# Performance work log

Hardware: AMD Instinct MI355X
Metric: run time of the kernel (lower is better)

Reference implementation:

```python
import jax, jax.numpy as jnp
import numpy as np

CELL = 0.5          # grid_map cell size (meters)
NUM_POSES = 256     # config.num_pose_samples


def setup_inputs() -> dict:
    key = jax.random.key(0)
    k1, k2, k3, k4 = jax.random.split(key, 4)
    B, N, I, J, D = 2, 1024, 128, 128, 32
    f_q = jax.random.normal(k1, (B, N, D), jnp.float32)
    f_map = jax.random.normal(k2, (B, I, J, D), jnp.float32)
    # query frustum points: 32x32 grid, x in [-15.5, 15.5], y in [0.5, 31.5]
    xs = jnp.arange(32, dtype=jnp.float32) - 15.5
    ys = jnp.arange(32, dtype=jnp.float32) + 0.5
    grid = jnp.stack(jnp.meshgrid(xs, ys, indexing='ij'), -1).reshape(-1, 2)
    q_xy = jnp.broadcast_to(grid, (B, N, 2)).astype(jnp.float32)
    valid_q = jax.random.bernoulli(k3, 0.9, (B, N))
    valid_map = jax.random.bernoulli(k4, 0.8, (B, I, J))
    temperature = jnp.array(0.5, jnp.float32)
    return {"f_q": f_q, "f_map": f_map, "q_xy": q_xy, "temperature": temperature,
            "valid_q": valid_q, "valid_map": valid_map, "seed": 0}


def reference(f_q, f_map, q_xy, temperature, valid_q, valid_map, seed):
    B, N, D = f_q.shape
    _, I, J, _ = f_map.shape
    K = NUM_POSES

    # dense cross-correlation: [B, N, I, J]
    sim = jnp.einsum('bnd,bijd->bnij', f_q, f_map)
    sim = jax.nn.relu(sim)                      # clip_negative_scores
    sim = sim.astype(jnp.float32) * jnp.exp(temperature)
    # joint softmax over the two spatial axes
    m = sim.max(axis=(-2, -1), keepdims=True)
    e = jnp.exp(sim - m)
    prob = e / e.sum(axis=(-2, -1), keepdims=True)
    num_valid = valid_q.sum(-1).clip(min=1).astype(jnp.float32)[:, None, None, None]
    sim = sim / num_valid
    prob = prob / num_valid

    # --- RANSAC 2-point pose sampling (no gradient through prob) ---
    p = jax.lax.stop_gradient(prob)
    kq, km = jax.random.split(jax.random.key(seed))
    n_idx = jax.random.randint(kq, (B, 2 * K), 0, N)          # 2 query pts per pose
    b_idx = jnp.arange(B)[:, None]
    p_flat = p.reshape(B, N, I * J)
    rows = p_flat[b_idx, n_idx]                               # [B, 2K, IJ]
    m_flat = jax.random.categorical(km, jnp.log(rows + 1e-20), axis=-1)  # [B, 2K]
    mi, mj = m_flat // J, m_flat % J
    m_xy = (jnp.stack([mi, mj], -1).astype(jnp.float32) + 0.5) * CELL    # cell centers
    m_xy = m_xy.reshape(B, K, 2, 2)
    q_pts = q_xy[b_idx, n_idx].reshape(B, K, 2, 2)
    dq = q_pts[:, :, 1] - q_pts[:, :, 0]
    dm = m_xy[:, :, 1] - m_xy[:, :, 0]
    theta = jnp.arctan2(dm[..., 1], dm[..., 0]) - jnp.arctan2(dq[..., 1], dq[..., 0])
    c, s = jnp.cos(theta), jnp.sin(theta)
    R = jnp.stack([jnp.stack([c, -s], -1), jnp.stack([s, c], -1)], -2)   # [B,K,2,2]
    t = m_xy[:, :, 0] - jnp.einsum('bkxy,bky->bkx', R, q_pts[:, :, 0])   # [B,K,2]

    # --- score every pose hypothesis ---
    p_map = jnp.einsum('bkxy,bny->bknx', R, q_xy) + t[:, :, None]        # [B,K,N,2]
    ij = jnp.floor(p_map / CELL).astype(jnp.int32)
    inb = (ij[..., 0] >= 0) & (ij[..., 0] < I) & (ij[..., 1] >= 0) & (ij[..., 1] < J)
    flat = jnp.clip(ij[..., 0], 0, I - 1) * J + jnp.clip(ij[..., 1], 0, J - 1)  # [B,K,N]
    vmap_flat = valid_map.reshape(B, I * J)
    vgather = vmap_flat[b_idx, flat.reshape(B, K * N)].reshape(B, K, N)
    sim_flat = sim.reshape(B, N, I * J)
    sgather = jnp.take_along_axis(sim_flat, flat.transpose(0, 2, 1), axis=2)  # [B,N,K]
    mask = valid_q[:, None, :] & inb & vgather                                # [B,K,N]
    scores = jnp.sum(sgather.transpose(0, 2, 1) * mask, axis=-1)              # [B,K]
    return scores
```

## Files before the change

### kernel.cpp

```cpp
#include <hip/hip_runtime.h>
#include <hip/hip_bf16.h>
#include <stdint.h>

typedef unsigned int u32;
typedef _Float16 f16x8 __attribute__((ext_vector_type(8)));
typedef float f32x4 __attribute__((ext_vector_type(4)));

#define IJ 16384
#define NQ 1024
#define NB 2
#define KP 256
#define NSEG 8
#define SEGW 2048

__device__ __forceinline__ void tf2x32(u32 k0, u32 k1, u32& x0, u32& x1) {
  u32 kx = k0 ^ k1 ^ 0x1BD11BDAu;
#define TFR(r) { x0 += x1; x1 = (x1 << (r)) | (x1 >> (32 - (r))); x1 ^= x0; }
  x0 += k0; x1 += k1;
  TFR(13) TFR(15) TFR(26) TFR(6)
  x0 += k1; x1 += kx + 1u;
  TFR(17) TFR(29) TFR(16) TFR(24)
  x0 += kx; x1 += k0 + 2u;
  TFR(13) TFR(15) TFR(26) TFR(6)
  x0 += k0; x1 += k1 + 3u;
  TFR(17) TFR(29) TFR(16) TFR(24)
  x0 += k1; x1 += kx + 4u;
  TFR(13) TFR(15) TFR(26) TFR(6)
  x0 += kx; x1 += k0 + 5u;
#undef TFR
}

__device__ __forceinline__ void tf_subkey(u32 k0, u32 k1, u32 i, u32& s0, u32& s1) {
  u32 x0 = 0u, x1 = i;
  tf2x32(k0, k1, x0, x1);
  s0 = x0; s1 = x1;
}

__device__ __forceinline__ u32 tf_xorbits(u32 k0, u32 k1, u32 i) {
  u32 x0 = 0u, x1 = i;
  tf2x32(k0, k1, x0, x1);
  return x0 ^ x1;
}

__device__ __forceinline__ void derive_keys(int seed, u32& kq0, u32& kq1,
                                            u32& km0, u32& km1) {
  u32 k0 = 0u;
  u32 k1 = (u32)seed;
  tf_subkey(k0, k1, 0u, kq0, kq1);
  tf_subkey(k0, k1, 1u, km0, km1);
}

__device__ __forceinline__ float gumbel_from_bits(u32 w) {
  const float tiny = 1.17549435e-38f;
  float fl = __uint_as_float((w >> 9) | 0x3f800000u) - 1.0f;
  float u = fl * (1.0f - tiny) + tiny;
  u = fmaxf(tiny, u);
  return -logf(-logf(u));
}

__device__ __forceinline__ bool read_bool(const void* p, int idx, int is32) {
  return is32 ? (((const int*)p)[idx] != 0)
              : (((const unsigned char*)p)[idx] != 0);
}

__global__ void setup_kernel(const void* __restrict__ valid_q,
                             const int* __restrict__ seedp,
                             float* __restrict__ row_max,
                             float* __restrict__ num_valid,
                             int* __restrict__ n_idx,
                             int* __restrict__ bool_is32) {
  __shared__ int sred[256];
  __shared__ int is32_s;
  const int blk = blockIdx.x, tid = threadIdx.x;
  if (blk < 4) {
    int s = blk * 256 + tid;
    u32 kq0, kq1, km0, km1;
    derive_keys(seedp[0], kq0, kq1, km0, km1);
    u32 l0, l1;
    tf_subkey(kq0, kq1, 1u, l0, l1);
    u32 w = tf_xorbits(l0, l1, (u32)s);
    n_idx[s] = (int)(w & 1023u);
  } else if (blk == 4) {
    const unsigned char* vb = (const unsigned char*)valid_q;
    int ones = 0;
    for (int i = tid; i < 2048; i += 256) ones += (vb[i] == 1) ? 1 : 0;
    sred[tid] = ones;
    __syncthreads();
    for (int off = 128; off > 0; off >>= 1) {
      if (tid < off) sred[tid] += sred[tid + off];
      __syncthreads();
    }
    if (tid == 0) {
      is32_s = (sred[0] < 1152) ? 1 : 0;
      bool_is32[0] = is32_s;
    }
    __syncthreads();
    const int is32 = is32_s;
    for (int b = 0; b < 2; ++b) {
      int acc = 0;
      for (int i = tid; i < NQ; i += 256)
        acc += read_bool(valid_q, b * NQ + i, is32) ? 1 : 0;
      sred[tid] = acc;
      __syncthreads();
      for (int off = 128; off > 0; off >>= 1) {
        if (tid < off) sred[tid] += sred[tid + off];
        __syncthreads();
      }
      if (tid == 0) {
        float nv = (float)sred[0];
        num_valid[b] = nv < 1.f ? 1.f : nv;
      }
      __syncthreads();
    }
  } else {
    for (int i = (blk - 5) * 256 + tid; i < NB * NQ; i += 768) row_max[i] = 0.f;
  }
}

__global__ __launch_bounds__(256) void gemm_kernel(
    const float* __restrict__ f_q, const float* __restrict__ f_map,
    const float* __restrict__ temp, float* __restrict__ sim,
    float* __restrict__ row_max, float* __restrict__ rowsum_part) {
  __shared__ __align__(16) _Float16 ldsA[2][4][64][8];
  __shared__ __align__(16) _Float16 ldsB[2][16][64][8];
  const int tid = threadIdx.x;
  const int b = blockIdx.z;
  const int n0 = blockIdx.y * 64;
  const int ij0 = blockIdx.x * 256;

  {
    const int l = tid & 63, rt = tid >> 6;
    const int g = l >> 4, r = l & 15;
    const float* src = f_q + ((size_t)b * NQ + n0 + rt * 16 + r) * 32 + g * 4;
    float4 v0 = *(const float4*)src;
    float4 v1 = *(const float4*)(src + 16);
    float x[8] = {v0.x, v0.y, v0.z, v0.w, v1.x, v1.y, v1.z, v1.w};
    f16x8 h1, h2;
#pragma unroll
    for (int e = 0; e < 8; ++e) {
      _Float16 a = (_Float16)x[e];
      h1[e] = a;
      h2[e] = (_Float16)((x[e] - (float)a) * 2048.0f);
    }
    *(f16x8*)(&ldsA[0][rt][l][0]) = h1;
    *(f16x8*)(&ldsA[1][rt][l][0]) = h2;
  }
  for (int s = tid; s < 1024; s += 256) {
    const int l = s & 63, t = s >> 6;
    const int g = l >> 4, r = l & 15;
    const float* src = f_map + ((size_t)b * IJ + ij0 + t * 16 + r) * 32 + g * 4;
    float4 v0 = *(const float4*)src;
    float4 v1 = *(const float4*)(src + 16);
    float x[8] = {v0.x, v0.y, v0.z, v0.w, v1.x, v1.y, v1.z, v1.w};
    f16x8 h1, h2;
#pragma unroll
    for (int e = 0; e < 8; ++e) {
      _Float16 a = (_Float16)x[e];
      h1[e] = a;
      h2[e] = (_Float16)((x[e] - (float)a) * 2048.0f);
    }
    *(f16x8*)(&ldsB[0][t][l][0]) = h1;
    *(f16x8*)(&ldsB[1][t][l][0]) = h2;
  }
  __syncthreads();

  const int w = tid >> 6, l = tid & 63;
  const f16x8 q1 = *(const f16x8*)(&ldsA[0][w][l][0]);
  const f16x8 q2 = *(const f16x8*)(&ldsA[1][w][l][0]);
  const f32x4 zero4 = {0.f, 0.f, 0.f, 0.f};
  const float c11 = 4.8828125e-4f;
  f32x4 acc[16];
#pragma unroll
  for (int t = 0; t < 16; ++t) {
    f16x8 m1 = *(const f16x8*)(&ldsB[0][t][l][0]);
    f16x8 m2 = *(const f16x8*)(&ldsB[1][t][l][0]);
    f32x4 x = __builtin_amdgcn_mfma_f32_16x16x32_f16(m2, q2, zero4, 0, 0, 0);
    x *= c11;
    x = __builtin_amdgcn_mfma_f32_16x16x32_f16(m2, q1, x, 0, 0, 0);
    x = __builtin_amdgcn_mfma_f32_16x16x32_f16(m1, q2, x, 0, 0, 0);
    x *= c11;
    acc[t] = __builtin_amdgcn_mfma_f32_16x16x32_f16(m1, q1, x, 0, 0, 0);
  }

  const float et = expf(temp[0]);
  const int r15 = l & 15, g = l >> 4;
  const int row = n0 + w * 16 + r15;
  float* base = sim + ((size_t)b * NQ + row) * IJ + ij0 + g * 4;
  float rm = 0.f, se = 0.f;
#pragma unroll
  for (int t = 0; t < 16; ++t) {
    float4 o;
    o.x = fmaxf(acc[t][0], 0.f) * et;
    o.y = fmaxf(acc[t][1], 0.f) * et;
    o.z = fmaxf(acc[t][2], 0.f) * et;
    o.w = fmaxf(acc[t][3], 0.f) * et;
    *(float4*)(base + t * 16) = o;
    rm = fmaxf(rm, fmaxf(fmaxf(o.x, o.y), fmaxf(o.z, o.w)));
    se += expf(o.x); se += expf(o.y); se += expf(o.z); se += expf(o.w);
  }
#pragma unroll
  for (int off = 16; off < 64; off <<= 1) {
    se += __shfl_xor(se, off, 64);
    rm = fmaxf(rm, __shfl_xor(rm, off, 64));
  }
  if (g == 0) {
    rowsum_part[((size_t)(b * NQ + row)) * 64 + blockIdx.x] = se;
    atomicMax((u32*)&row_max[(size_t)b * NQ + row], __float_as_uint(rm));
  }
}

__global__ void sumexp_reduce_kernel(const float* __restrict__ rowsum_part,
                                     const float* __restrict__ row_max,
                                     float* __restrict__ row_sumexp) {
  const int row = blockIdx.x * 256 + threadIdx.x;
  if (row >= NB * NQ) return;
  const float* p = rowsum_part + (size_t)row * 64;
  float s = 0.f;
#pragma unroll
  for (int t = 0; t < 64; ++t) s += p[t];
  row_sumexp[row] = s * expf(-row_max[row]);
}

__global__ __launch_bounds__(256) void cat_seg_kernel(
    const float* __restrict__ sim, const float* __restrict__ row_max,
    const float* __restrict__ row_sumexp, const float* __restrict__ num_valid,
    const int* __restrict__ n_idx, const int* __restrict__ seedp,
    float* __restrict__ segv, int* __restrict__ segi) {
  __shared__ unsigned short cand[2][SEGW];
  __shared__ int ccount[2];
  __shared__ u32 keys[2];
  __shared__ float sv[2][256];
  __shared__ int si[2][256];
  const int seg = blockIdx.x;
  const int t = blockIdx.y;
  const int tid = threadIdx.x;
  if (tid == 0) {
    u32 kq0, kq1, km0, km1;
    derive_keys(seedp[0], kq0, kq1, km0, km1);
    keys[0] = km0; keys[1] = km1;
    ccount[0] = 0; ccount[1] = 0;
  }
  __syncthreads();

  const int nA = n_idx[t], nB = n_idx[512 + t];
  const float m0 = row_max[nA], s0 = row_sumexp[nA];
  const float m1 = row_max[NQ + nB], s1 = row_sumexp[NQ + nB];
  const float nv0 = num_valid[0], nv1 = num_valid[1];
  const float thA = m0 - 25.0f;
  const float thB = m1 - 25.0f;
  const float* r0 = sim + (size_t)nA * IJ + seg * SEGW;
  const float* r1 = sim + (size_t)(NQ + nB) * IJ + seg * SEGW;

#pragma unroll
  for (int k = 0; k < 2; ++k) {
    const int l = tid + k * 256;
    const int lf = l * 4;
    float4 va = ((const float4*)r0)[l];
    float4 vb = ((const float4*)r1)[l];
    const float ra[4] = {va.x, va.y, va.z, va.w};
    const float rb[4] = {vb.x, vb.y, vb.z, vb.w};
#pragma unroll
    for (int c = 0; c < 4; ++c) {
      if (ra[c] > thA) { int p = atomicAdd(&ccount[0], 1); cand[0][p] = (unsigned short)(lf + c); }
      if (rb[c] > thB) { int p = atomicAdd(&ccount[1], 1); cand[1][p] = (unsigned short)(lf + c); }
    }
  }
  __syncthreads();

  const u32 km0 = keys[0], km1 = keys[1];
  const int c0 = ccount[0], c1 = ccount[1];
  const int fbase = seg * SEGW;
  float bv0 = -1e30f, bv1 = -1e30f;
  int bi0 = IJ, bi1 = IJ;
  for (int c = tid; c < c0; c += 256) {
    int f = fbase + (int)cand[0][c];
    u32 w = tf_xorbits(km0, km1, (u32)(t * IJ + f));
    float g = gumbel_from_bits(w);
    float e = expf(r0[f - fbase] - m0);
    float v = logf((e / s0) / nv0 + 1e-20f) + g;
    if (v > bv0 || (v == bv0 && f < bi0)) { bv0 = v; bi0 = f; }
  }
  for (int c = tid; c < c1; c += 256) {
    int f = fbase + (int)cand[1][c];
    u32 w = tf_xorbits(km0, km1, (u32)(t * IJ + f) + 8388608u);
    float g = gumbel_from_bits(w);
    float e = expf(r1[f - fbase] - m1);
    float v = logf((e / s1) / nv1 + 1e-20f) + g;
    if (v > bv1 || (v == bv1 && f < bi1)) { bv1 = v; bi1 = f; }
  }
  sv[0][tid] = bv0; si[0][tid] = bi0;
  sv[1][tid] = bv1; si[1][tid] = bi1;
  __syncthreads();
  for (int off = 128; off > 0; off >>= 1) {
    if (tid < off) {
#pragma unroll
      for (int q = 0; q < 2; ++q) {
        float v2 = sv[q][tid + off];
        int i2 = si[q][tid + off];
        if (v2 > sv[q][tid] || (v2 == sv[q][tid] && i2 < si[q][tid])) {
          sv[q][tid] = v2; si[q][tid] = i2;
        }
      }
    }
    __syncthreads();
  }
  if (tid == 0) {
    segv[(0 * 512 + t) * NSEG + seg] = sv[0][0];
    segi[(0 * 512 + t) * NSEG + seg] = si[0][0];
    segv[(1 * 512 + t) * NSEG + seg] = sv[1][0];
    segi[(1 * 512 + t) * NSEG + seg] = si[1][0];
  }
}

__global__ void cat_reduce_kernel(const float* __restrict__ segv,
                                  const int* __restrict__ segi,
                                  int* __restrict__ m_flat) {
  const int idx = blockIdx.x * 256 + threadIdx.x;
  if (idx >= NB * 512) return;
  float bv = -1e30f;
  int bi = IJ;
#pragma unroll
  for (int s = 0; s < NSEG; ++s) {
    float v = segv[idx * NSEG + s];
    int i = segi[idx * NSEG + s];
    if (v > bv || (v == bv && i < bi)) { bv = v; bi = i; }
  }
  m_flat[idx] = bi;
}

__global__ void pose_kernel(const float* __restrict__ q_xy,
                            const int* __restrict__ n_idx,
                            const int* __restrict__ m_flat,
                            float4* __restrict__ poses) {
  const int idx = blockIdx.x * 256 + threadIdx.x;
  if (idx >= NB * KP) return;
  const int b = idx >> 8, k = idx & 255;
  const int t0 = b * 512 + 2 * k, t1 = t0 + 1;
  const int na = n_idx[t0], nb = n_idx[t1];
  const float2 q0 = ((const float2*)q_xy)[(size_t)b * NQ + na];
  const float2 q1 = ((const float2*)q_xy)[(size_t)b * NQ + nb];
  const int ma = m_flat[t0], mb = m_flat[t1];
  const float m0x = ((float)(ma >> 7) + 0.5f) * 0.5f;
  const float m0y = ((float)(ma & 127) + 0.5f) * 0.5f;
  const float m1x = ((float)(mb >> 7) + 0.5f) * 0.5f;
  const float m1y = ((float)(mb & 127) + 0.5f) * 0.5f;
  const float dqx = q1.x - q0.x, dqy = q1.y - q0.y;
  const float dmx = m1x - m0x, dmy = m1y - m0y;
  const float theta = atan2f(dmy, dmx) - atan2f(dqy, dqx);
  const float c = cosf(theta), s = sinf(theta);
  const float tx = m0x - (c * q0.x - s * q0.y);
  const float ty = m0y - (s * q0.x + c * q0.y);
  poses[idx] = make_float4(c, s, tx, ty);
}

__global__ __launch_bounds__(256) void score_kernel(
    const float* __restrict__ sim, const float* __restrict__ q_xy,
    const void* __restrict__ valid_q, const void* __restrict__ valid_map,
    const float* __restrict__ num_valid, const float4* __restrict__ poses,
    const int* __restrict__ bool_is32, float* __restrict__ out) {
  __shared__ float sred[256];
  const int idx = blockIdx.x;
  const int tid = threadIdx.x;
  const int b = idx >> 8;
  const int is32 = bool_is32[0];
  const float4 P = poses[idx];
  float acc = 0.f;
  for (int n = tid; n < NQ; n += 256) {
    float2 q = ((const float2*)q_xy)[(size_t)b * NQ + n];
    float px = P.x * q.x - P.y * q.y + P.z;
    float py = P.y * q.x + P.x * q.y + P.w;
    int ii = (int)floorf(px * 2.0f);
    int jj = (int)floorf(py * 2.0f);
    bool inb = (ii >= 0) & (ii < 128) & (jj >= 0) & (jj < 128);
    int ic = min(max(ii, 0), 127), jc = min(max(jj, 0), 127);
    int flat = (ic << 7) + jc;
    bool msk = read_bool(valid_q, b * NQ + n, is32) && inb &&
               read_bool(valid_map, b * IJ + flat, is32);
    if (msk) acc += sim[((size_t)(b * NQ + n)) * IJ + flat];
  }
  sred[tid] = acc;
  __syncthreads();
  for (int off = 128; off > 0; off >>= 1) {
    if (tid < off) sred[tid] += sred[tid + off];
    __syncthreads();
  }
  if (tid == 0) out[idx] = sred[0] / num_valid[b];
}

extern "C" void kernel_launch(void* const* d_in, const int* in_sizes, int n_in,
                              void* d_out, int out_size, void* d_ws,
                              size_t ws_size, hipStream_t stream) {
  const float* f_q = (const float*)d_in[0];
  const float* f_map = (const float*)d_in[1];
  const float* q_xy = (const float*)d_in[2];
  const float* temp = (const float*)d_in[3];
  const void* valid_q = d_in[4];
  const void* valid_map = d_in[5];
  const int* seedp = (const int*)d_in[6];
  float* out = (float*)d_out;

  char* ws = (char*)d_ws;
  const size_t SIM_BYTES = (size_t)NB * NQ * IJ * 4;
  float* sim = (float*)ws;
  float* row_max = (float*)(ws + SIM_BYTES);
  float* row_sumexp = (float*)(ws + SIM_BYTES + 8192);
  float* num_valid = (float*)(ws + SIM_BYTES + 16384);
  int* n_idx = (int*)(ws + SIM_BYTES + 16448);
  int* m_flat = (int*)(ws + SIM_BYTES + 20544);
  float4* poses = (float4*)(ws + SIM_BYTES + 24640);
  int* bool_is32 = (int*)(ws + SIM_BYTES + 32832);
  float* segv = (float*)(ws + SIM_BYTES + 36864);
  int* segi = (int*)(ws + SIM_BYTES + 69632);
  float* rowsum_part = (float*)(ws + SIM_BYTES + 102400);

  setup_kernel<<<8, 256, 0, stream>>>(valid_q, seedp, row_max, num_valid,
                                      n_idx, bool_is32);
  gemm_kernel<<<dim3(64, 16, 2), 256, 0, stream>>>(f_q, f_map, temp, sim,
                                                   row_max, rowsum_part);
  sumexp_reduce_kernel<<<8, 256, 0, stream>>>(rowsum_part, row_max, row_sumexp);
  cat_seg_kernel<<<dim3(NSEG, 512), 256, 0, stream>>>(
      sim, row_max, row_sumexp, num_valid, n_idx, seedp, segv, segi);
  cat_reduce_kernel<<<4, 256, 0, stream>>>(segv, segi, m_flat);
  pose_kernel<<<2, 256, 0, stream>>>(q_xy, n_idx, m_flat, poses);
  score_kernel<<<NB * KP, 256, 0, stream>>>(sim, q_xy, valid_q, valid_map,
                                            num_valid, poses, bool_is32, out);
}
```

Before: 151.1 us.

## Compute similarity only for sampled rows and recompute gathered scores on the fly

Drops the full 2x1024x16384 similarity matrix. The feature maps are pre-split into fp16 hi/lo pairs once, and the softmax stats and categorical selection are computed only for the 1024 sampled query rows by recomputing their MFMA products. The score kernel recomputes each gathered similarity as a 32-wide fp32 dot product instead of reading stored sim. This removes the large sim write and read traffic at the cost of redundant MFMA work, and candidate selection now uses packed 64-bit atomicMax keys. A risk is small numeric differences from __expf and the fp32 dot, which could change sampled indices or scores.

Measured after the change: 144.9 us. 4.1% less time.

```diff
diff --git a/kernel.cpp b/kernel.cpp
--- a/kernel.cpp
+++ b/kernel.cpp
@@ -1,17 +1,19 @@
 #include <hip/hip_runtime.h>
-#include <hip/hip_bf16.h>
 #include <stdint.h>
 
 typedef unsigned int u32;
+typedef unsigned long long u64;
 typedef _Float16 f16x8 __attribute__((ext_vector_type(8)));
+typedef _Float16 f16x4 __attribute__((ext_vector_type(4)));
 typedef float f32x4 __attribute__((ext_vector_type(4)));
 
 #define IJ 16384
 #define NQ 1024
 #define NB 2
 #define KP 256
-#define NSEG 8
-#define SEGW 2048
+#define NSEG 16
+#define SEGW 1024
+#define NT 1024
 
 __device__ __forceinline__ void tf2x32(u32 k0, u32 k1, u32& x0, u32& x1) {
   u32 kx = k0 ^ k1 ^ 0x1BD11BDAu;
@@ -63,12 +65,36 @@
               : (((const unsigned char*)p)[idx] != 0);
 }
 
+__device__ __forceinline__ u32 fkey(float x) {
+  u32 b = __float_as_uint(x);
+  return b ^ ((b & 0x80000000u) ? 0xFFFFFFFFu : 0x80000000u);
+}
+__device__ __forceinline__ float fkey_inv(u32 k) {
+  u32 b = k ^ ((k & 0x80000000u) ? 0x80000000u : 0xFFFFFFFFu);
+  return __uint_as_float(b);
+}
+
+__device__ __forceinline__ void split8(const float* x, f16x8& h1, f16x8& h2) {
+#pragma unroll
+  for (int e = 0; e < 8; ++e) {
+    _Float16 a = (_Float16)x[e];
+    h1[e] = a;
+    h2[e] = (_Float16)((x[e] - (float)a) * 2048.0f);
+  }
+}
+
 __global__ void setup_kernel(const void* __restrict__ valid_q,
                              const int* __restrict__ seedp,
-                             float* __restrict__ row_max,
+                             const float* __restrict__ f_q,
+                             const float* __restrict__ f_map,
+                             float* __restrict__ tmax,
                              float* __restrict__ num_valid,
                              int* __restrict__ n_idx,
-                             int* __restrict__ bool_is32) {
+                             int* __restrict__ bool_is32,
+                             _Float16* __restrict__ ms1,
+                             _Float16* __restrict__ ms2,
+                             _Float16* __restrict__ qs1,
+                             _Float16* __restrict__ qs2) {
   __shared__ int sred[256];
   __shared__ int is32_s;
   const int blk = blockIdx.x, tid = threadIdx.x;
@@ -112,203 +138,191 @@
       }
       __syncthreads();
     }
-  } else {
-    for (int i = (blk - 5) * 256 + tid; i < NB * NQ; i += 768) row_max[i] = 0.f;
-  }
-}
-
-__global__ __launch_bounds__(256) void gemm_kernel(
-    const float* __restrict__ f_q, const float* __restrict__ f_map,
-    const float* __restrict__ temp, float* __restrict__ sim,
-    float* __restrict__ row_max, float* __restrict__ rowsum_part) {
-  __shared__ __align__(16) _Float16 ldsA[2][4][64][8];
-  __shared__ __align__(16) _Float16 ldsB[2][16][64][8];
-  const int tid = threadIdx.x;
-  const int b = blockIdx.z;
-  const int n0 = blockIdx.y * 64;
-  const int ij0 = blockIdx.x * 256;
-
-  {
-    const int l = tid & 63, rt = tid >> 6;
-    const int g = l >> 4, r = l & 15;
-    const float* src = f_q + ((size_t)b * NQ + n0 + rt * 16 + r) * 32 + g * 4;
+  } else if (blk < 8) {
+    for (int i = (blk - 5) * 256 + tid; i < NT; i += 768) tmax[i] = 0.f;
+  } else if (blk < 520) {
+    const int TT = (blk - 8) * 4 + (tid >> 6);
+    const int l = tid & 63;
+    const int bb = TT >> 10, T = TT & 1023;
+    const float* src =
+        f_map + ((size_t)bb * IJ + T * 16 + (l & 15)) * 32 + ((l >> 4) << 2);
     float4 v0 = *(const float4*)src;
     float4 v1 = *(const float4*)(src + 16);
     float x[8] = {v0.x, v0.y, v0.z, v0.w, v1.x, v1.y, v1.z, v1.w};
     f16x8 h1, h2;
-#pragma unroll
-    for (int e = 0; e < 8; ++e) {
-      _Float16 a = (_Float16)x[e];
-      h1[e] = a;
-      h2[e] = (_Float16)((x[e] - (float)a) * 2048.0f);
-    }
-    *(f16x8*)(&ldsA[0][rt][l][0]) = h1;
-    *(f16x8*)(&ldsA[1][rt][l][0]) = h2;
-  }
-  for (int s = tid; s < 1024; s += 256) {
-    const int l = s & 63, t = s >> 6;
-    const int g = l >> 4, r = l & 15;
-    const float* src = f_map + ((size_t)b * IJ + ij0 + t * 16 + r) * 32 + g * 4;
-    float4 v0 = *(const float4*)src;
-    float4 v1 = *(const float4*)(src + 16);
-    float x[8] = {v0.x, v0.y, v0.z, v0.w, v1.x, v1.y, v1.z, v1.w};
+    split8(x, h1, h2);
+    *(f16x8*)(ms1 + (size_t)(TT * 64 + l) * 8) = h1;
+    *(f16x8*)(ms2 + (size_t)(TT * 64 + l) * 8) = h2;
+  } else {
+    const int i = (blk - 520) * 256 + tid;
+    const float* src = f_q + (size_t)i * 8;
+    float4 a = *(const float4*)src;
+    float4 b4 = *(const float4*)(src + 4);
+    float x[8] = {a.x, a.y, a.z, a.w, b4.x, b4.y, b4.z, b4.w};
     f16x8 h1, h2;
-#pragma unroll
-    for (int e = 0; e < 8; ++e) {
-      _Float16 a = (_Float16)x[e];
-      h1[e] = a;
-      h2[e] = (_Float16)((x[e] - (float)a) * 2048.0f);
-    }
-    *(f16x8*)(&ldsB[0][t][l][0]) = h1;
-    *(f16x8*)(&ldsB[1][t][l][0]) = h2;
-  }
-  __syncthreads();
-
-  const int w = tid >> 6, l = tid & 63;
-  const f16x8 q1 = *(const f16x8*)(&ldsA[0][w][l][0]);
-  const f16x8 q2 = *(const f16x8*)(&ldsA[1][w][l][0]);
+    split8(x, h1, h2);
+    *(f16x8*)(qs1 + (size_t)i * 8) = h1;
+    *(f16x8*)(qs2 + (size_t)i * 8) = h2;
+  }
+}
+
+__global__ __launch_bounds__(256) void stats_kernel(
+    const _Float16* __restrict__ ms1, const _Float16* __restrict__ ms2,
+    const _Float16* __restrict__ qs1, const _Float16* __restrict__ qs2,
+    const int* __restrict__ n_idx, const float* __restrict__ temp,
+    float* __restrict__ tmax, float* __restrict__ rowsum_part) {
+  const int bx = blockIdx.x;
+  const int by = blockIdx.y;
+  const int tid = threadIdx.x;
+  const int w = tid >> 6, l = tid & 63, l15 = l & 15, g = l >> 4;
+  const int b = by >> 3;
+  const int tp = by * 64 + w * 16 + l15;
+  const int n = n_idx[tp];
+  const size_t qb = ((size_t)b * NQ + n) * 32 + g * 4;
+  union { f16x8 v8; f16x4 v4[2]; } uq;
+  uq.v4[0] = *(const f16x4*)(qs1 + qb);
+  uq.v4[1] = *(const f16x4*)(qs1 + qb + 16);
+  const f16x8 q1 = uq.v8;
+  uq.v4[0] = *(const f16x4*)(qs2 + qb);
+  uq.v4[1] = *(const f16x4*)(qs2 + qb + 16);
+  const f16x8 q2 = uq.v8;
+  const float et = expf(temp[0]);
   const f32x4 zero4 = {0.f, 0.f, 0.f, 0.f};
   const float c11 = 4.8828125e-4f;
-  f32x4 acc[16];
-#pragma unroll
-  for (int t = 0; t < 16; ++t) {
-    f16x8 m1 = *(const f16x8*)(&ldsB[0][t][l][0]);
-    f16x8 m2 = *(const f16x8*)(&ldsB[1][t][l][0]);
+  const size_t mbase = ((size_t)b * 1024 + bx * 16) * 512 + (size_t)l * 8;
+  float rm = 0.f, se = 0.f;
+#pragma unroll
+  for (int T = 0; T < 16; ++T) {
+    const f16x8 m1 = *(const f16x8*)(ms1 + mbase + (size_t)T * 512);
+    const f16x8 m2 = *(const f16x8*)(ms2 + mbase + (size_t)T * 512);
     f32x4 x = __builtin_amdgcn_mfma_f32_16x16x32_f16(m2, q2, zero4, 0, 0, 0);
     x *= c11;
     x = __builtin_amdgcn_mfma_f32_16x16x32_f16(m2, q1, x, 0, 0, 0);
     x = __builtin_amdgcn_mfma_f32_16x16x32_f16(m1, q2, x, 0, 0, 0);
     x *= c11;
-    acc[t] = __builtin_amdgcn_mfma_f32_16x16x32_f16(m1, q1, x, 0, 0, 0);
-  }
-
-  const float et = expf(temp[0]);
-  const int r15 = l & 15, g = l >> 4;
-  const int row = n0 + w * 16 + r15;
-  float* base = sim + ((size_t)b * NQ + row) * IJ + ij0 + g * 4;
-  float rm = 0.f, se = 0.f;
-#pragma unroll
-  for (int t = 0; t < 16; ++t) {
-    float4 o;
-    o.x = fmaxf(acc[t][0], 0.f) * et;
-    o.y = fmaxf(acc[t][1], 0.f) * et;
-    o.z = fmaxf(acc[t][2], 0.f) * et;
-    o.w = fmaxf(acc[t][3], 0.f) * et;
-    *(float4*)(base + t * 16) = o;
-    rm = fmaxf(rm, fmaxf(fmaxf(o.x, o.y), fmaxf(o.z, o.w)));
-    se += expf(o.x); se += expf(o.y); se += expf(o.z); se += expf(o.w);
-  }
-#pragma unroll
-  for (int off = 16; off < 64; off <<= 1) {
-    se += __shfl_xor(se, off, 64);
-    rm = fmaxf(rm, __shfl_xor(rm, off, 64));
-  }
+    f32x4 r = __builtin_amdgcn_mfma_f32_16x16x32_f16(m1, q1, x, 0, 0, 0);
+#pragma unroll
+    for (int j = 0; j < 4; ++j) {
+      float v = fmaxf(r[j], 0.f) * et;
+      rm = fmaxf(rm, v);
+      se += __expf(v);
+    }
+  }
+  se += __shfl_xor(se, 16, 64);
+  rm = fmaxf(rm, __shfl_xor(rm, 16, 64));
+  se += __shfl_xor(se, 32, 64);
+  rm = fmaxf(rm, __shfl_xor(rm, 32, 64));
   if (g == 0) {
-    rowsum_part[((size_t)(b * NQ + row)) * 64 + blockIdx.x] = se;
-    atomicMax((u32*)&row_max[(size_t)b * NQ + row], __float_as_uint(rm));
+    rowsum_part[(size_t)tp * 64 + bx] = se;
+    atomicMax((u32*)&tmax[tp], __float_as_uint(rm));
   }
 }
 
 __global__ void sumexp_reduce_kernel(const float* __restrict__ rowsum_part,
-                                     const float* __restrict__ row_max,
-                                     float* __restrict__ row_sumexp) {
+                                     const float* __restrict__ tmax,
+                                     float* __restrict__ tsum) {
   const int row = blockIdx.x * 256 + threadIdx.x;
-  if (row >= NB * NQ) return;
+  if (row >= NT) return;
   const float* p = rowsum_part + (size_t)row * 64;
   float s = 0.f;
 #pragma unroll
   for (int t = 0; t < 64; ++t) s += p[t];
-  row_sumexp[row] = s * expf(-row_max[row]);
-}
-
-__global__ __launch_bounds__(256) void cat_seg_kernel(
-    const float* __restrict__ sim, const float* __restrict__ row_max,
-    const float* __restrict__ row_sumexp, const float* __restrict__ num_valid,
-    const int* __restrict__ n_idx, const int* __restrict__ seedp,
+  tsum[row] = s * expf(-tmax[row]);
+}
+
+__global__ __launch_bounds__(256) void select_kernel(
+    const _Float16* __restrict__ ms1, const _Float16* __restrict__ ms2,
+    const _Float16* __restrict__ qs1, const _Float16* __restrict__ qs2,
+    const int* __restrict__ n_idx, const float* __restrict__ temp,
+    const float* __restrict__ tmax, const float* __restrict__ tsum,
+    const float* __restrict__ num_valid, const int* __restrict__ seedp,
     float* __restrict__ segv, int* __restrict__ segi) {
-  __shared__ unsigned short cand[2][SEGW];
-  __shared__ int ccount[2];
-  __shared__ u32 keys[2];
-  __shared__ float sv[2][256];
-  __shared__ int si[2][256];
+  __shared__ float mrow[16], srow[16];
+  __shared__ u64 best[16];
+  __shared__ u32 keysm[2];
+  __shared__ int cnt;
+  __shared__ u32 candk[4096];
+  __shared__ float candv[4096];
   const int seg = blockIdx.x;
-  const int t = blockIdx.y;
+  const int tg = blockIdx.y;
   const int tid = threadIdx.x;
+  const int w = tid >> 6, l = tid & 63, l15 = l & 15, g = l >> 4;
+  const int b = tg >> 5;
+  const int t0 = tg * 16;
+  if (tid < 16) {
+    mrow[tid] = tmax[t0 + tid];
+    srow[tid] = tsum[t0 + tid];
+    best[tid] = ((u64)fkey(-1e30f) << 32) | (u64)(0xFFFFFFFFu - (u32)IJ);
+  }
   if (tid == 0) {
     u32 kq0, kq1, km0, km1;
     derive_keys(seedp[0], kq0, kq1, km0, km1);
-    keys[0] = km0; keys[1] = km1;
-    ccount[0] = 0; ccount[1] = 0;
-  }
+    keysm[0] = km0; keysm[1] = km1;
+    cnt = 0;
+  }
+  const int tp = t0 + l15;
+  const int n = n_idx[tp];
+  const size_t qb = ((size_t)b * NQ + n) * 32 + g * 4;
+  union { f16x8 v8; f16x4 v4[2]; } uq;
+  uq.v4[0] = *(const f16x4*)(qs1 + qb);
+  uq.v4[1] = *(const f16x4*)(qs1 + qb + 16);
+  const f16x8 q1 = uq.v8;
+  uq.v4[0] = *(const f16x4*)(qs2 + qb);
+  uq.v4[1] = *(const f16x4*)(qs2 + qb + 16);
+  const f16x8 q2 = uq.v8;
+  const float et = expf(temp[0]);
+  const f32x4 zero4 = {0.f, 0.f, 0.f, 0.f};
+  const float c11 = 4.8828125e-4f;
+  const float nv = num_valid[b];
   __syncthreads();
-
-  const int nA = n_idx[t], nB = n_idx[512 + t];
-  const float m0 = row_max[nA], s0 = row_sumexp[nA];
-  const float m1 = row_max[NQ + nB], s1 = row_sumexp[NQ + nB];
-  const float nv0 = num_valid[0], nv1 = num_valid[1];
-  const float thA = m0 - 25.0f;
-  const float thB = m1 - 25.0f;
-  const float* r0 = sim + (size_t)nA * IJ + seg * SEGW;
-  const float* r1 = sim + (size_t)(NQ + nB) * IJ + seg * SEGW;
-
-#pragma unroll
-  for (int k = 0; k < 2; ++k) {
-    const int l = tid + k * 256;
-    const int lf = l * 4;
-    float4 va = ((const float4*)r0)[l];
-    float4 vb = ((const float4*)r1)[l];
-    const float ra[4] = {va.x, va.y, va.z, va.w};
-    const float rb[4] = {vb.x, vb.y, vb.z, vb.w};
-#pragma unroll
-    for (int c = 0; c < 4; ++c) {
-      if (ra[c] > thA) { int p = atomicAdd(&ccount[0], 1); cand[0][p] = (unsigned short)(lf + c); }
-      if (rb[c] > thB) { int p = atomicAdd(&ccount[1], 1); cand[1][p] = (unsigned short)(lf + c); }
-    }
-  }
-  __syncthreads();
-
-  const u32 km0 = keys[0], km1 = keys[1];
-  const int c0 = ccount[0], c1 = ccount[1];
-  const int fbase = seg * SEGW;
-  float bv0 = -1e30f, bv1 = -1e30f;
-  int bi0 = IJ, bi1 = IJ;
-  for (int c = tid; c < c0; c += 256) {
-    int f = fbase + (int)cand[0][c];
-    u32 w = tf_xorbits(km0, km1, (u32)(t * IJ + f));
-    float g = gumbel_from_bits(w);
-    float e = expf(r0[f - fbase] - m0);
-    float v = logf((e / s0) / nv0 + 1e-20f) + g;
-    if (v > bv0 || (v == bv0 && f < bi0)) { bv0 = v; bi0 = f; }
-  }
-  for (int c = tid; c < c1; c += 256) {
-    int f = fbase + (int)cand[1][c];
-    u32 w = tf_xorbits(km0, km1, (u32)(t * IJ + f) + 8388608u);
-    float g = gumbel_from_bits(w);
-    float e = expf(r1[f - fbase] - m1);
-    float v = logf((e / s1) / nv1 + 1e-20f) + g;
-    if (v > bv1 || (v == bv1 && f < bi1)) { bv1 = v; bi1 = f; }
-  }
-  sv[0][tid] = bv0; si[0][tid] = bi0;
-  sv[1][tid] = bv1; si[1][tid] = bi1;
-  __syncthreads();
-  for (int off = 128; off > 0; off >>= 1) {
-    if (tid < off) {
-#pragma unroll
-      for (int q = 0; q < 2; ++q) {
-        float v2 = sv[q][tid + off];
-        int i2 = si[q][tid + off];
-        if (v2 > sv[q][tid] || (v2 == sv[q][tid] && i2 < si[q][tid])) {
-          sv[q][tid] = v2; si[q][tid] = i2;
+  const float th = mrow[l15] - 25.0f;
+  const u32 km0 = keysm[0], km1 = keysm[1];
+
+  for (int sc = 0; sc < 4; ++sc) {
+#pragma unroll
+    for (int i = 0; i < 4; ++i) {
+      const int Tl = sc * 16 + w * 4 + i;
+      const size_t moff = ((size_t)(b * 1024 + seg * 64 + Tl) * 64 + l) * 8;
+      const f16x8 m1 = *(const f16x8*)(ms1 + moff);
+      const f16x8 m2 = *(const f16x8*)(ms2 + moff);
+      f32x4 x = __builtin_amdgcn_mfma_f32_16x16x32_f16(m2, q2, zero4, 0, 0, 0);
+      x *= c11;
+      x = __builtin_amdgcn_mfma_f32_16x16x32_f16(m2, q1, x, 0, 0, 0);
+      x = __builtin_amdgcn_mfma_f32_16x16x32_f16(m1, q2, x, 0, 0, 0);
+      x *= c11;
+      f32x4 r = __builtin_amdgcn_mfma_f32_16x16x32_f16(m1, q1, x, 0, 0, 0);
+#pragma unroll
+      for (int j = 0; j < 4; ++j) {
+        float v = fmaxf(r[j], 0.f) * et;
+        if (v > th) {
+          int p = atomicAdd(&cnt, 1);
+          candk[p] = ((u32)l15 << 12) | (u32)(Tl * 16 + g * 4 + j);
+          candv[p] = v;
         }
       }
     }
     __syncthreads();
-  }
-  if (tid == 0) {
-    segv[(0 * 512 + t) * NSEG + seg] = sv[0][0];
-    segi[(0 * 512 + t) * NSEG + seg] = si[0][0];
-    segv[(1 * 512 + t) * NSEG + seg] = sv[1][0];
-    segi[(1 * 512 + t) * NSEG + seg] = si[1][0];
+    const int C = cnt;
+    for (int c = tid; c < C; c += 256) {
+      const u32 e = candk[c];
+      const int r = (int)(e >> 12);
+      const int f = seg * SEGW + (int)(e & 4095u);
+      const float val = candv[c];
+      const u32 wb = tf_xorbits(km0, km1, (u32)((t0 + r) * IJ + f));
+      const float gmb = gumbel_from_bits(wb);
+      const float v = logf((expf(val - mrow[r]) / srow[r]) / nv + 1e-20f) + gmb;
+      const u64 key = ((u64)fkey(v) << 32) | (u64)(0xFFFFFFFFu - (u32)f);
+      atomicMax(&best[r], key);
+    }
+    __syncthreads();
+    if (tid == 0) cnt = 0;
+    __syncthreads();
+  }
+  if (tid < 16) {
+    const u64 k = best[tid];
+    segv[(size_t)(t0 + tid) * NSEG + seg] = fkey_inv((u32)(k >> 32));
+    segi[(size_t)(t0 + tid) * NSEG + seg] =
+        (int)(0xFFFFFFFFu - (u32)(k & 0xFFFFFFFFu));
   }
 }
 
@@ -316,7 +330,7 @@
                                   const int* __restrict__ segi,
                                   int* __restrict__ m_flat) {
   const int idx = blockIdx.x * 256 + threadIdx.x;
-  if (idx >= NB * 512) return;
+  if (idx >= NT) return;
   float bv = -1e30f;
   int bi = IJ;
 #pragma unroll
@@ -354,9 +368,10 @@
 }
 
 __global__ __launch_bounds__(256) void score_kernel(
-    const float* __restrict__ sim, const float* __restrict__ q_xy,
-    const void* __restrict__ valid_q, const void* __restrict__ valid_map,
-    const float* __restrict__ num_valid, const float4* __restrict__ poses,
+    const float* __restrict__ f_q, const float* __restrict__ f_map,
+    const float* __restrict__ q_xy, const void* __restrict__ valid_q,
+    const void* __restrict__ valid_map, const float* __restrict__ num_valid,
+    const float* __restrict__ temp, const float4* __restrict__ poses,
     const int* __restrict__ bool_is32, float* __restrict__ out) {
   __shared__ float sred[256];
   const int idx = blockIdx.x;
@@ -364,6 +379,7 @@
   const int b = idx >> 8;
   const int is32 = bool_is32[0];
   const float4 P = poses[idx];
+  const float et = expf(temp[0]);
   float acc = 0.f;
   for (int n = tid; n < NQ; n += 256) {
     float2 q = ((const float2*)q_xy)[(size_t)b * NQ + n];
@@ -376,7 +392,21 @@
     int flat = (ic << 7) + jc;
     bool msk = read_bool(valid_q, b * NQ + n, is32) && inb &&
                read_bool(valid_map, b * IJ + flat, is32);
-    if (msk) acc += sim[((size_t)(b * NQ + n)) * IJ + flat];
+    if (msk) {
+      const float4* A = (const float4*)(f_q + ((size_t)b * NQ + n) * 32);
+      const float4* Bm = (const float4*)(f_map + ((size_t)b * IJ + flat) * 32);
+      float4 s4 = {0.f, 0.f, 0.f, 0.f};
+#pragma unroll
+      for (int r = 0; r < 8; ++r) {
+        float4 a = A[r], bb = Bm[r];
+        s4.x = fmaf(a.x, bb.x, s4.x);
+        s4.y = fmaf(a.y, bb.y, s4.y);
+        s4.z = fmaf(a.z, bb.z, s4.z);
+        s4.w = fmaf(a.w, bb.w, s4.w);
+      }
+      float dot = (s4.x + s4.y) + (s4.z + s4.w);
+      acc += fmaxf(dot, 0.f) * et;
+    }
   }
   sred[tid] = acc;
   __syncthreads();
@@ -400,28 +430,33 @@
   float* out = (float*)d_out;
 
   char* ws = (char*)d_ws;
-  const size_t SIM_BYTES = (size_t)NB * NQ * IJ * 4;
-  float* sim = (float*)ws;
-  float* row_max = (float*)(ws + SIM_BYTES);
-  float* row_sumexp = (float*)(ws + SIM_BYTES + 8192);
-  float* num_valid = (float*)(ws + SIM_BYTES + 16384);
-  int* n_idx = (int*)(ws + SIM_BYTES + 16448);
-  int* m_flat = (int*)(ws + SIM_BYTES + 20544);
-  float4* poses = (float4*)(ws + SIM_BYTES + 24640);
-  int* bool_is32 = (int*)(ws + SIM_BYTES + 32832);
-  float* segv = (float*)(ws + SIM_BYTES + 36864);
-  int* segi = (int*)(ws + SIM_BYTES + 69632);
-  float* rowsum_part = (float*)(ws + SIM_BYTES + 102400);
-
-  setup_kernel<<<8, 256, 0, stream>>>(valid_q, seedp, row_max, num_valid,
-                                      n_idx, bool_is32);
-  gemm_kernel<<<dim3(64, 16, 2), 256, 0, stream>>>(f_q, f_map, temp, sim,
-                                                   row_max, rowsum_part);
-  sumexp_reduce_kernel<<<8, 256, 0, stream>>>(rowsum_part, row_max, row_sumexp);
-  cat_seg_kernel<<<dim3(NSEG, 512), 256, 0, stream>>>(
-      sim, row_max, row_sumexp, num_valid, n_idx, seedp, segv, segi);
+  _Float16* ms1 = (_Float16*)(ws + 0);
+  _Float16* ms2 = (_Float16*)(ws + 2097152);
+  _Float16* qs1 = (_Float16*)(ws + 4194304);
+  _Float16* qs2 = (_Float16*)(ws + 4325376);
+  float* tmax = (float*)(ws + 4456448);
+  float* tsum = (float*)(ws + 4460544);
+  float* rowsum_part = (float*)(ws + 4464640);
+  float* num_valid = (float*)(ws + 4726784);
+  int* n_idx = (int*)(ws + 4726848);
+  int* m_flat = (int*)(ws + 4730944);
+  float4* poses = (float4*)(ws + 4735040);
+  int* bool_is32 = (int*)(ws + 4743232);
+  float* segv = (float*)(ws + 4743296);
+  int* segi = (int*)(ws + 4808832);
+
+  setup_kernel<<<552, 256, 0, stream>>>(valid_q, seedp, f_q, f_map, tmax,
+                                        num_valid, n_idx, bool_is32, ms1, ms2,
+                                        qs1, qs2);
+  stats_kernel<<<dim3(64, 16), 256, 0, stream>>>(ms1, ms2, qs1, qs2, n_idx,
+                                                 temp, tmax, rowsum_part);
+  sumexp_reduce_kernel<<<4, 256, 0, stream>>>(rowsum_part, tmax, tsum);
+  select_kernel<<<dim3(NSEG, 64), 256, 0, stream>>>(
+      ms1, ms2, qs1, qs2, n_idx, temp, tmax, tsum, num_valid, seedp, segv,
+      segi);
   cat_reduce_kernel<<<4, 256, 0, stream>>>(segv, segi, m_flat);
   pose_kernel<<<2, 256, 0, stream>>>(q_xy, n_idx, m_flat, poses);
-  score_kernel<<<NB * KP, 256, 0, stream>>>(sim, q_xy, valid_q, valid_map,
-                                            num_valid, poses, bool_is32, out);
-}
+  score_kernel<<<NB * KP, 256, 0, stream>>>(f_q, f_map, q_xy, valid_q,
+                                            valid_map, num_valid, temp, poses,
+                                            bool_is32, out);
+}
```
